# Performance work log

Hardware: AMD Instinct MI355X
Metric: run time of the kernel (lower is better)

The kernel has to match this reference:

```python
import jax, jax.numpy as jnp
import numpy as np

B, L, INPUT_DIM = 2, 2048, 512
D_MODEL, N_HEAD, MLP_HIDDEN = 1024, 16, 4096
CONTEXT_LENGTH = 2048
EPS = 1e-5


def _layer_norm(x, w, b):
    mu = jnp.mean(x, axis=-1, keepdims=True)
    var = jnp.mean(jnp.square(x - mu), axis=-1, keepdims=True)
    return (x - mu) * jax.lax.rsqrt(var + EPS) * w + b


def setup_inputs() -> dict:
    key = jax.random.key(0)
    ks = jax.random.split(key, 12)
    s = 0.02
    return {
        "x": jax.random.normal(ks[0], (B, L, INPUT_DIM), dtype=jnp.float32),
        "wte_w": jax.random.normal(ks[1], (INPUT_DIM, D_MODEL), dtype=jnp.float32) * s,
        "wte_b": jnp.zeros((D_MODEL,), dtype=jnp.float32),
        "wpe": jax.random.normal(ks[2], (CONTEXT_LENGTH, D_MODEL), dtype=jnp.float32) * s,
        "ln1_w": jnp.ones((D_MODEL,), dtype=jnp.float32),
        "ln1_b": jnp.zeros((D_MODEL,), dtype=jnp.float32),
        "kq_w": jax.random.normal(ks[3], (D_MODEL, 2 * D_MODEL), dtype=jnp.float32) * s,
        "kq_b": jnp.zeros((2 * D_MODEL,), dtype=jnp.float32),
        "v_w": jax.random.normal(ks[4], (D_MODEL, D_MODEL), dtype=jnp.float32) * s,
        "v_b": jnp.zeros((D_MODEL,), dtype=jnp.float32),
        "ao_w": jax.random.normal(ks[5], (D_MODEL, D_MODEL), dtype=jnp.float32) * s,
        "ao_b": jnp.zeros((D_MODEL,), dtype=jnp.float32),
        "ln2_w": jnp.ones((D_MODEL,), dtype=jnp.float32),
        "ln2_b": jnp.zeros((D_MODEL,), dtype=jnp.float32),
        "fc_w": jax.random.normal(ks[6], (D_MODEL, MLP_HIDDEN), dtype=jnp.float32) * s,
        "fc_b": jnp.zeros((MLP_HIDDEN,), dtype=jnp.float32),
        "proj_w": jax.random.normal(ks[7], (MLP_HIDDEN, INPUT_DIM), dtype=jnp.float32) * s,
        "proj_b": jnp.zeros((INPUT_DIM,), dtype=jnp.float32),
    }


def reference(x, wte_w, wte_b, wpe, ln1_w, ln1_b, kq_w, kq_b, v_w, v_b,
              ao_w, ao_b, ln2_w, ln2_b, fc_w, fc_b, proj_w, proj_b):
    b, l, _ = x.shape
    hd = D_MODEL // N_HEAD
    # token "embedding" (linear) + learnable positional embedding
    h = x @ wte_w + wte_b + wpe[:l]                      # [B, L, D]
    hn = _layer_norm(h, ln1_w, ln1_b)                    # ln_1
    # attention (kq fused linear -> split gives k first, then q)
    kq = hn @ kq_w + kq_b                                # [B, L, 2D]
    k, q = kq[..., :D_MODEL], kq[..., D_MODEL:]
    v = hn @ v_w + v_b
    q = q.reshape(b, l, N_HEAD, hd).transpose(0, 2, 1, 3)  # [B, H, L, hd]
    k = k.reshape(b, l, N_HEAD, hd).transpose(0, 2, 1, 3)
    v = v.reshape(b, l, N_HEAD, hd).transpose(0, 2, 1, 3)
    scale = 1.0 / jnp.sqrt(jnp.asarray(hd, dtype=q.dtype))
    scores = jnp.einsum('bhqd,bhkd->bhqk', q, k) * scale  # [B, H, L, L]
    causal = jnp.tril(jnp.ones((l, l), dtype=bool))
    scores = jnp.where(causal, scores, jnp.asarray(-jnp.inf, dtype=scores.dtype))
    attn = jax.nn.softmax(scores, axis=-1)
    o = jnp.einsum('bhqk,bhkd->bhqd', attn, v)            # [B, H, L, hd]
    o = o.transpose(0, 2, 1, 3).reshape(b, l, D_MODEL)
    o = o @ ao_w + ao_b
    attn_out = hn + o                                     # residual recorded by Block
    xo = _layer_norm(attn_out, ln2_w, ln2_b)              # ln_2
    # MLP head to input_dim (exact GELU, matching torch nn.GELU default)
    out = jax.nn.gelu(xo @ fc_w + fc_b, approximate=False) @ proj_w + proj_b
    return (out, attn_out)
```

## Files before the change

### kernel.cpp

```cpp
#include <hip/hip_runtime.h>
#include <hip/hip_bf16.h>
#include <cmath>

#define D_MODEL   1024
#define N_HEAD    16
#define HEAD_DIM  64
#define SEQ_LEN   2048
#define NBATCH    2
#define M_TOTAL   (NBATCH * SEQ_LEN)
#define IN_DIM    512
#define MLP_HID   4096

typedef __attribute__((ext_vector_type(8))) short short8;
typedef __attribute__((ext_vector_type(4))) short short4v;
typedef __attribute__((ext_vector_type(4))) float floatx4;

typedef const __attribute__((address_space(1))) void* gas_ptr;
typedef __attribute__((address_space(3))) void* las_ptr;

__device__ __forceinline__ void async_copy16(const void* g, void* l) {
  __builtin_amdgcn_global_load_lds((gas_ptr)g, (las_ptr)l, 16, 0, 0);
}


__global__ __launch_bounds__(256) void k_prep(const float* __restrict__ wte_w,
                                              const float* __restrict__ kq_w,
                                              const float* __restrict__ v_w,
                                              const float* __restrict__ ao_w,
                                              const float* __restrict__ fc_w,
                                              const float* __restrict__ proj_w,
                                              const float* __restrict__ x,
                                              __hip_bfloat16* __restrict__ wT,
                                              __hip_bfloat16* __restrict__ x_bf) {
  const int bid = blockIdx.x;
  const float* in; __hip_bfloat16* out; int K, N, local;
  if (bid < 512)        { in = wte_w;  out = wT;           K = IN_DIM;  N = D_MODEL;     local = bid;        }
  else if (bid < 2560)  { in = kq_w;   out = wT +  524288; K = D_MODEL; N = 2 * D_MODEL; local = bid - 512;  }
  else if (bid < 3584)  { in = v_w;    out = wT + 2621440; K = D_MODEL; N = D_MODEL;     local = bid - 2560; }
  else if (bid < 4608)  { in = ao_w;   out = wT + 3670016; K = D_MODEL; N = D_MODEL;     local = bid - 3584; }
  else if (bid < 8704)  { in = fc_w;   out = wT + 4718592; K = D_MODEL; N = MLP_HID;     local = bid - 4608; }
  else if (bid < 10752) { in = proj_w; out = wT + 8912896; K = MLP_HID; N = IN_DIM;      local = bid - 8704; }
  else {
    int i = (bid - 10752) * 256 + threadIdx.x;
    float4 v = ((const float4*)x)[i];
    short4v o;
    ((__hip_bfloat16*)&o)[0] = __float2bfloat16(v.x);
    ((__hip_bfloat16*)&o)[1] = __float2bfloat16(v.y);
    ((__hip_bfloat16*)&o)[2] = __float2bfloat16(v.z);
    ((__hip_bfloat16*)&o)[3] = __float2bfloat16(v.w);
    ((short4v*)x_bf)[i] = o;
    return;
  }
  __shared__ float tile[32][33];
  const int ntx = N >> 5;
  const int bx = local % ntx, by = local / ntx;
  const int n0 = bx * 32, k0 = by * 32;
  const int tx = threadIdx.x & 31, ty = threadIdx.x >> 5;
#pragma unroll
  for (int i = 0; i < 32; i += 8)
    tile[ty + i][tx] = in[(size_t)(k0 + ty + i) * N + n0 + tx];
  __syncthreads();
#pragma unroll
  for (int i = 0; i < 32; i += 8)
    out[(size_t)(n0 + ty + i) * K + k0 + tx] = __float2bfloat16(tile[tx][ty + i]);
}

__global__ __launch_bounds__(256) void k_reduce_proj(const __hip_bfloat16* __restrict__ part,
                                                     const float* __restrict__ bias,
                                                     float* __restrict__ out) {
  int i = blockIdx.x * 256 + threadIdx.x;
  const size_t SP = (size_t)M_TOTAL * IN_DIM / 4;
  float4 s = ((const float4*)bias)[i & (IN_DIM / 4 - 1)];
#pragma unroll
  for (int j = 0; j < 8; j++) {
    short4v v = ((const short4v*)part)[i + j * SP];
    s.x += __bfloat162float(((const __hip_bfloat16*)&v)[0]);
    s.y += __bfloat162float(((const __hip_bfloat16*)&v)[1]);
    s.z += __bfloat162float(((const __hip_bfloat16*)&v)[2]);
    s.w += __bfloat162float(((const __hip_bfloat16*)&v)[3]);
  }
  ((float4*)out)[i] = s;
}


__global__ __launch_bounds__(256) void k_ln1_combine(const float* __restrict__ part,
                                                     const float* __restrict__ wb,
                                                     const float* __restrict__ wpe,
                                                     const float* __restrict__ lw,
                                                     const float* __restrict__ lb,
                                                     __hip_bfloat16* __restrict__ out_bf) {
  int row = blockIdx.x;
  int l = row & (SEQ_LEN - 1);
  float4 a = ((const float4*)(part + (size_t)row * D_MODEL))[threadIdx.x];
  float4 c = ((const float4*)(part + (size_t)(M_TOTAL + row) * D_MODEL))[threadIdx.x];
  float4 wb4 = ((const float4*)wb)[threadIdx.x];
  float4 pe4 = ((const float4*)(wpe + (size_t)l * D_MODEL))[threadIdx.x];
  float4 v;
  v.x = a.x + c.x + wb4.x + pe4.x;
  v.y = a.y + c.y + wb4.y + pe4.y;
  v.z = a.z + c.z + wb4.z + pe4.z;
  v.w = a.w + c.w + wb4.w + pe4.w;
  float s  = v.x + v.y + v.z + v.w;
  float sq = v.x * v.x + v.y * v.y + v.z * v.z + v.w * v.w;
#pragma unroll
  for (int o = 1; o < 64; o <<= 1) { s += __shfl_xor(s, o); sq += __shfl_xor(sq, o); }
  __shared__ float ss[4], ssq[4];
  int lane = threadIdx.x & 63, wv = threadIdx.x >> 6;
  if (lane == 0) { ss[wv] = s; ssq[wv] = sq; }
  __syncthreads();
  s  = ss[0] + ss[1] + ss[2] + ss[3];
  sq = ssq[0] + ssq[1] + ssq[2] + ssq[3];
  float mu  = s * (1.f / D_MODEL);
  float var = sq * (1.f / D_MODEL) - mu * mu;
  float rs  = rsqrtf(var + 1e-5f);
  float4 lw4 = ((const float4*)lw)[threadIdx.x];
  float4 lb4 = ((const float4*)lb)[threadIdx.x];
  size_t base = (size_t)row * D_MODEL + threadIdx.x * 4;
  out_bf[base + 0] = __float2bfloat16((v.x - mu) * rs * lw4.x + lb4.x);
  out_bf[base + 1] = __float2bfloat16((v.y - mu) * rs * lw4.y + lb4.y);
  out_bf[base + 2] = __float2bfloat16((v.z - mu) * rs * lw4.z + lb4.z);
  out_bf[base + 3] = __float2bfloat16((v.w - mu) * rs * lw4.w + lb4.w);
}

__global__ __launch_bounds__(256) void k_ln2_combine(const float* __restrict__ part,
                                                     const float* __restrict__ bias,
                                                     const __hip_bfloat16* __restrict__ hn,
                                                     const float* __restrict__ lw,
                                                     const float* __restrict__ lb,
                                                     float* __restrict__ attn_out,
                                                     __hip_bfloat16* __restrict__ out_bf) {
  int row = blockIdx.x;
  float4 a = ((const float4*)(part + (size_t)row * D_MODEL))[threadIdx.x];
  float4 c = ((const float4*)(part + (size_t)(M_TOTAL + row) * D_MODEL))[threadIdx.x];
  float4 b4 = ((const float4*)bias)[threadIdx.x];
  short4v h4 = ((const short4v*)(hn + (size_t)row * D_MODEL))[threadIdx.x];
  float4 v;
  v.x = a.x + c.x + b4.x + __bfloat162float(((const __hip_bfloat16*)&h4)[0]);
  v.y = a.y + c.y + b4.y + __bfloat162float(((const __hip_bfloat16*)&h4)[1]);
  v.z = a.z + c.z + b4.z + __bfloat162float(((const __hip_bfloat16*)&h4)[2]);
  v.w = a.w + c.w + b4.w + __bfloat162float(((const __hip_bfloat16*)&h4)[3]);
  ((float4*)(attn_out + (size_t)row * D_MODEL))[threadIdx.x] = v;
  float s  = v.x + v.y + v.z + v.w;
  float sq = v.x * v.x + v.y * v.y + v.z * v.z + v.w * v.w;
#pragma unroll
  for (int o = 1; o < 64; o <<= 1) { s += __shfl_xor(s, o); sq += __shfl_xor(sq, o); }
  __shared__ float ss[4], ssq[4];
  int lane = threadIdx.x & 63, wv = threadIdx.x >> 6;
  if (lane == 0) { ss[wv] = s; ssq[wv] = sq; }
  __syncthreads();
  s  = ss[0] + ss[1] + ss[2] + ss[3];
  sq = ssq[0] + ssq[1] + ssq[2] + ssq[3];
  float mu  = s * (1.f / D_MODEL);
  float var = sq * (1.f / D_MODEL) - mu * mu;
  float rs  = rsqrtf(var + 1e-5f);
  float4 lw4 = ((const float4*)lw)[threadIdx.x];
  float4 lb4 = ((const float4*)lb)[threadIdx.x];
  size_t base = (size_t)row * D_MODEL + threadIdx.x * 4;
  out_bf[base + 0] = __float2bfloat16((v.x - mu) * rs * lw4.x + lb4.x);
  out_bf[base + 1] = __float2bfloat16((v.y - mu) * rs * lw4.y + lb4.y);
  out_bf[base + 2] = __float2bfloat16((v.z - mu) * rs * lw4.z + lb4.z);
  out_bf[base + 3] = __float2bfloat16((v.w - mu) * rs * lw4.w + lb4.w);
}


struct KQVEpi {
  const float* kq_b; const float* v_b;
  __hip_bfloat16* kb; __hip_bfloat16* qb; __hip_bfloat16* vt;
  __device__ void operator()(int row, int col, const floatx4& v) const {
    int b = row >> 11, l = row & (SEQ_LEN - 1);
    int which = col >> 10, c = col & (D_MODEL - 1);
    int head = c >> 6, d = c & 63;
    if (which == 2) {
      float bias = v_b[c];
      short4v o;
#pragma unroll
      for (int t = 0; t < 4; t++)
        ((__hip_bfloat16*)&o)[t] = __float2bfloat16(v[t] + bias);
      *(short4v*)(vt + ((size_t)(b * N_HEAD + head) * HEAD_DIM + d) * SEQ_LEN + l) = o;
    } else {
      float bias = kq_b[col];
      float scale = (which == 1) ? 0.125f : 1.f;
      __hip_bfloat16* dst = (which == 0) ? kb : qb;
#pragma unroll
      for (int t = 0; t < 4; t++)
        dst[((size_t)(b * N_HEAD + head) * SEQ_LEN + l + t) * HEAD_DIM + d] =
            __float2bfloat16((v[t] + bias) * scale);
    }
  }
};

struct FCEpi {
  const float* bias; __hip_bfloat16* act;
  __device__ void operator()(int row, int col, const floatx4& v) const {
    float bi = bias[col];
#pragma unroll
    for (int t = 0; t < 4; t++) {
      float x = v[t] + bi;
      float g = 0.5f * x * (1.f + erff(x * 0.70710678118654752f));
      act[(size_t)(row + t) * MLP_HID + col] = __float2bfloat16(g);
    }
  }
};

struct PartEpi {
  float* part;
  __device__ void operator()(int row, int col, const floatx4& v) const {
    float* p = part + (size_t)blockIdx.z * ((size_t)M_TOTAL * D_MODEL) +
               (size_t)row * D_MODEL + col;
#pragma unroll
    for (int t = 0; t < 4; t++) p[(size_t)t * D_MODEL] = v[t];
  }
};

struct PartBf16Epi {
  __hip_bfloat16* part;
  __device__ void operator()(int row, int col, const floatx4& v) const {
    __hip_bfloat16* p = part + (size_t)blockIdx.z * ((size_t)M_TOTAL * IN_DIM) +
                        (size_t)row * IN_DIM + col;
#pragma unroll
    for (int t = 0; t < 4; t++) p[(size_t)t * IN_DIM] = __float2bfloat16(v[t]);
  }
};


template <class Epi>
__global__ __launch_bounds__(256) void k_gemm(const __hip_bfloat16* __restrict__ A,
                                              const __hip_bfloat16* __restrict__ Bt,
                                              int M, int N, int K, int Kchunk, Epi epi) {
  __shared__ __align__(16) short As[128 * 64];
  __shared__ __align__(16) short Bs[128 * 64];
  const int tid  = threadIdx.x;
  const int lane = tid & 63;
  const int w    = tid >> 6;
  const int wm   = (w >> 1) << 6;
  const int wn   = (w & 1) << 6;
  const int r    = lane & 15;
  const int quad = lane >> 4;
  const int m0 = blockIdx.y << 7;
  const int n0 = blockIdx.x << 7;
  const int koff = blockIdx.z * Kchunk;

  const __hip_bfloat16* pa[4];
  const __hip_bfloat16* pb[4];
#pragma unroll
  for (int j = 0; j < 4; j++) {
    int s = tid + j * 256;
    int row = s >> 3;
    int c = (s & 7) ^ (row & 7);
    pa[j] = A  + (size_t)(m0 + row) * K + (c << 3) + koff;
    pb[j] = Bt + (size_t)(n0 + row) * K + (c << 3) + koff;
  }

  floatx4 acc[4][4];
#pragma unroll
  for (int i = 0; i < 4; i++)
#pragma unroll
    for (int j = 0; j < 4; j++) acc[i][j] = (floatx4){0.f, 0.f, 0.f, 0.f};

  int aoff[2][4], boff[2][4];
#pragma unroll
  for (int kk = 0; kk < 2; kk++)
#pragma unroll
    for (int i = 0; i < 4; i++) {
      int pc = ((quad + (kk << 2)) ^ (r & 7)) << 3;
      aoff[kk][i] = (wm + i * 16 + r) * 64 + pc;
      boff[kk][i] = (wn + i * 16 + r) * 64 + pc;
    }

  for (int k0 = 0; k0 < Kchunk; k0 += 64) {
    __syncthreads();
#pragma unroll
    for (int j = 0; j < 4; j++) {
      async_copy16(pa[j] + k0, &As[(tid + j * 256) * 8]);
      async_copy16(pb[j] + k0, &Bs[(tid + j * 256) * 8]);
    }
    __syncthreads();
#pragma unroll
    for (int kk = 0; kk < 2; kk++) {
      short8 fa[4], fb[4];
#pragma unroll
      for (int i = 0; i < 4; i++) {
        fa[i] = *(const short8*)&As[aoff[kk][i]];
        fb[i] = *(const short8*)&Bs[boff[kk][i]];
      }
#pragma unroll
      for (int i = 0; i < 4; i++)
#pragma unroll
        for (int j = 0; j < 4; j++)
          acc[i][j] = __builtin_amdgcn_mfma_f32_16x16x32_bf16(fa[i], fb[j], acc[i][j], 0, 0, 0);
    }
  }

#pragma unroll
  for (int i = 0; i < 4; i++)
#pragma unroll
    for (int j = 0; j < 4; j++)
      epi(m0 + wm + i * 16 + quad * 4, n0 + wn + j * 16 + r, acc[i][j]);
}

template <class Epi>
static void launch_gemm(const __hip_bfloat16* A, const __hip_bfloat16* Bt,
                        int M, int N, int K, Epi epi, hipStream_t s) {
  dim3 grid(N / 128, M / 128, 1);
  k_gemm<Epi><<<grid, 256, 0, s>>>(A, Bt, M, N, K, K, epi);
}


#define STAGE_A(BUF, H, KT)                                                       \
  do {                                                                            \
    async_copy16(ga + (size_t)((H) * 128) * K + (KT) * 64,                        \
                 &As[BUF][(tid + (H) * 1024) * 8]);                               \
    async_copy16(ga + (size_t)((H) * 128 + 64) * K + (KT) * 64,                   \
                 &As[BUF][(tid + (H) * 1024 + 512) * 8]);                         \
  } while (0)

#define STAGE_B(BUF, H, KT)                                                       \
  do {                                                                            \
    async_copy16(gb + (size_t)((H) * 128) * K + (KT) * 64,                        \
                 &Bs[BUF][(tid + (H) * 1024) * 8]);                               \
    async_copy16(gb + (size_t)((H) * 128 + 64) * K + (KT) * 64,                   \
                 &Bs[BUF][(tid + (H) * 1024 + 512) * 8]);                         \
  } while (0)

#define MFMA_BLK(IO, JO, BFX)                                                     \
  _Pragma("unroll") for (int i = 0; i < 4; i++) {                                 \
    _Pragma("unroll") for (int j = 0; j < 2; j++) {                               \
      acc[(IO) + i][(JO) + j] = __builtin_amdgcn_mfma_f32_16x16x32_bf16(          \
          af[i][0], BFX[j][0], acc[(IO) + i][(JO) + j], 0, 0, 0);                 \
      acc[(IO) + i][(JO) + j] = __builtin_amdgcn_mfma_f32_16x16x32_bf16(          \
          af[i][1], BFX[j][1], acc[(IO) + i][(JO) + j], 0, 0, 0);                 \
    }                                                                             \
  }

#define GTILE(T, BUF)                                                             \
  {                                                                               \
    _Pragma("unroll") for (int i = 0; i < 4; i++) {                               \
      af[i][0] = *(const short8*)&As[BUF][arb[i] + pc0];                          \
      af[i][1] = *(const short8*)&As[BUF][arb[i] + pc1];                          \
    }                                                                             \
    _Pragma("unroll") for (int j = 0; j < 2; j++) {                               \
      bf0[j][0] = *(const short8*)&Bs[BUF][brb[j] + pc0];                         \
      bf0[j][1] = *(const short8*)&Bs[BUF][brb[j] + pc1];                         \
    }                                                                             \
    if ((T) + 1 < nt) { STAGE_A((BUF) ^ 1, 1, (T) + 1); }                         \
    __builtin_amdgcn_s_barrier();                                                 \
    asm volatile("s_waitcnt lgkmcnt(0)" ::: "memory");                            \
    __builtin_amdgcn_s_setprio(1);                                                \
    MFMA_BLK(0, 0, bf0)                                                           \
    __builtin_amdgcn_s_setprio(0);                                                \
    __builtin_amdgcn_s_barrier();                                                 \
    _Pragma("unroll") for (int j = 0; j < 2; j++) {                               \
      bf1[j][0] = *(const short8*)&Bs[BUF][brb[j] + 8192 + pc0];                  \
      bf1[j][1] = *(const short8*)&Bs[BUF][brb[j] + 8192 + pc1];                  \
    }                                                                             \
    if ((T) + 2 < nt) { STAGE_A(BUF, 0, (T) + 2); }                               \
    __builtin_amdgcn_s_barrier();                                                 \
    asm volatile("s_waitcnt lgkmcnt(0)" ::: "memory");                            \
    __builtin_amdgcn_s_setprio(1);                                                \
    MFMA_BLK(0, 2, bf1)                                                           \
    __builtin_amdgcn_s_setprio(0);                                                \
    __builtin_amdgcn_s_barrier();                                                 \
    _Pragma("unroll") for (int i = 0; i < 4; i++) {                               \
      af[i][0] = *(const short8*)&As[BUF][arb[i] + 8192 + pc0];                   \
      af[i][1] = *(const short8*)&As[BUF][arb[i] + 8192 + pc1];                   \
    }                                                                             \
    if ((T) + 2 < nt) { STAGE_B(BUF, 0, (T) + 2); }                               \
    __builtin_amdgcn_s_barrier();                                                 \
    asm volatile("s_waitcnt lgkmcnt(0)" ::: "memory");                            \
    __builtin_amdgcn_s_setprio(1);                                                \
    MFMA_BLK(4, 0, bf0)                                                           \
    __builtin_amdgcn_s_setprio(0);                                                \
    __builtin_amdgcn_s_barrier();                                                 \
    if ((T) + 2 < nt) { STAGE_B(BUF, 1, (T) + 2); }                               \
    __builtin_amdgcn_s_setprio(1);                                                \
    MFMA_BLK(4, 2, bf1)                                                           \
    __builtin_amdgcn_s_setprio(0);                                                \
    if ((T) + 2 < nt) {                                                           \
      asm volatile("s_waitcnt vmcnt(6)" ::: "memory");                            \
    } else {                                                                      \
      asm volatile("s_waitcnt vmcnt(0)" ::: "memory");                            \
    }                                                                             \
    __builtin_amdgcn_s_barrier();                                                 \
  }

template <class Epi>
__global__ __launch_bounds__(512, 2) void k_gemm256(const __hip_bfloat16* __restrict__ A,
                                                    const __hip_bfloat16* __restrict__ Bt,
                                                    int M, int N, int K, int Kchunk, Epi epi) {
  (void)M; (void)N;
  __shared__ __align__(16) short As[2][16384];
  __shared__ __align__(16) short Bs[2][16384];
  const int tid  = threadIdx.x;
  const int lane = tid & 63;
  const int w    = tid >> 6;
  const int wr   = w >> 2;
  const int wc   = w & 3;
  const int r    = lane & 15;
  const int quad = lane >> 4;
  const int m0 = blockIdx.y << 8;
  const int n0 = blockIdx.x << 8;
  const int koff = blockIdx.z * Kchunk;
  const int nt = Kchunk >> 6;

  const int sr = tid >> 3;
  const int sc = (tid & 7) ^ (sr & 7);
  const __hip_bfloat16* ga = A  + (size_t)(m0 + sr) * K + sc * 8 + koff;
  const __hip_bfloat16* gb = Bt + (size_t)(n0 + sr) * K + sc * 8 + koff;

  const int pc0 = ((quad    ) ^ (r & 7)) << 3;
  const int pc1 = ((quad + 4) ^ (r & 7)) << 3;
  int arb[4], brb[2];
#pragma unroll
  for (int i = 0; i < 4; i++) arb[i] = ((2 * i + wr) * 16 + r) * 64;
#pragma unroll
  for (int j = 0; j < 2; j++) brb[j] = ((4 * j + wc) * 16 + r) * 64;

  floatx4 acc[8][4];
#pragma unroll
  for (int i = 0; i < 8; i++)
#pragma unroll
    for (int j = 0; j < 4; j++) acc[i][j] = (floatx4){0.f, 0.f, 0.f, 0.f};
  short8 af[4][2], bf0[2][2], bf1[2][2];

  STAGE_A(0, 0, 0);
  STAGE_B(0, 0, 0);
  STAGE_B(0, 1, 0);
  STAGE_A(0, 1, 0);
  if (nt > 1) {
    STAGE_A(1, 0, 1);
    STAGE_B(1, 0, 1);
    STAGE_B(1, 1, 1);
    asm volatile("s_waitcnt vmcnt(6)" ::: "memory");
  } else {
    asm volatile("s_waitcnt vmcnt(0)" ::: "memory");
  }
  __builtin_amdgcn_s_barrier();

  for (int t = 0; t < nt; t += 2) {
    GTILE(t, 0)
    GTILE(t + 1, 1)
  }

#pragma unroll
  for (int i = 0; i < 8; i++)
#pragma unroll
    for (int j = 0; j < 4; j++)
      epi(m0 + (2 * i + wr) * 16 + quad * 4, n0 + (4 * j + wc) * 16 + r, acc[i][j]);
}


#define PSTR 68

#define STAGE_KV(T, P)                                                         \
  do {                                                                         \
    async_copy16(kp + (size_t)((((T) << 6)) + srow) * HEAD_DIM + sg * 8,       \
                 &Ks[P][tid * 8]);                                             \
    async_copy16(vp + (size_t)srow * SEQ_LEN + ((T) << 6) + sg * 8,            \
                 &Vs[P][tid * 8]);                                             \
  } while (0)

#define ATILE(T, P)                                                            \
  {                                                                            \
    const int ts = (T) << 6;                                                   \
    if (ts < qend) {                                                           \
      _Pragma("unroll") for (int kt = 0; kt < 4; kt++) {                       \
        const int tss = ts + (kt << 4);                                        \
        short4v pk0;                                                           \
        if (tss < qend) {                                                      \
          const int krow = (kt << 4) + r;                                      \
          short8 a0 = *(const short8*)&Ks[P][(krow * 8 + (quad ^ sw)) * 8];    \
          short8 a1 = *(const short8*)&Ks[P][(krow * 8 + ((quad ^ sw) ^ 4)) * 8]; \
          floatx4 s0 = (floatx4){0.f, 0.f, 0.f, 0.f};                          \
          s0 = __builtin_amdgcn_mfma_f32_16x16x32_bf16(a0, qf0, s0, 0, 0, 0);  \
          s0 = __builtin_amdgcn_mfma_f32_16x16x32_bf16(a1, qf1, s0, 0, 0, 0);  \
          if (tss + 15 > qbw) {                                                \
            int off0 = qbw + r - tss;                                          \
            _Pragma("unroll") for (int tt = 0; tt < 4; tt++) {                 \
              int kl = (quad << 2) + tt;                                       \
              if (kl > off0) s0[tt] = -INFINITY;                               \
            }                                                                  \
          }                                                                    \
          _Pragma("unroll") for (int tt = 0; tt < 4; tt++) {                   \
            float e0 = __expf(s0[tt]); ls0 += e0;                              \
            ((__hip_bfloat16*)&pk0)[tt] = __float2bfloat16(e0);                \
          }                                                                    \
        } else {                                                               \
          pk0 = (short4v){0, 0, 0, 0};                                         \
        }                                                                      \
        *(short4v*)(pw + r * PSTR + (kt << 4) + (quad << 2)) = pk0;            \
      }                                                                        \
      __builtin_amdgcn_s_setprio(1);                                           \
      _Pragma("unroll") for (int c = 0; c < 2; c++) {                          \
        short8 pb0 = *(const short8*)(pw + r * PSTR + (c << 5) + (quad << 3)); \
        _Pragma("unroll") for (int fd = 0; fd < 4; fd++) {                     \
          const int vrow = (fd << 4) + r;                                      \
          short8 va = *(const short8*)&Vs[P][(vrow * 8 + (((c << 2) + quad) ^ sw)) * 8]; \
          of[fd] = __builtin_amdgcn_mfma_f32_16x16x32_bf16(va, pb0, of[fd], 0, 0, 0); \
        }                                                                      \
      }                                                                        \
      __builtin_amdgcn_s_setprio(0);                                           \
    }                                                                          \
    __builtin_amdgcn_s_barrier();                                              \
    if ((T) + 2 < ktiles) {                                                    \
      STAGE_KV((T) + 2, P);                                                    \
      asm volatile("s_waitcnt vmcnt(2)" ::: "memory");                         \
    } else {                                                                   \
      asm volatile("s_waitcnt vmcnt(0)" ::: "memory");                         \
    }                                                                          \
    __builtin_amdgcn_s_barrier();                                              \
    __builtin_amdgcn_sched_barrier(0);                                         \
  }

__global__ __launch_bounds__(512, 4) void k_flash_attn(const __hip_bfloat16* __restrict__ kb,
                                                       const __hip_bfloat16* __restrict__ qb,
                                                       const __hip_bfloat16* __restrict__ vtb,
                                                       __hip_bfloat16* __restrict__ ob) {
  __shared__ __align__(16) short Ks[2][64 * 64];
  __shared__ __align__(16) short Vs[2][64 * 64];
  __shared__ __align__(16) __hip_bfloat16 Pb[8][16 * PSTR];
  const int tid  = threadIdx.x;
  const int lane = tid & 63;
  const int w    = tid >> 6;
  const int r    = lane & 15;
  const int quad = lane >> 4;
  const int sw   = r & 7;
  const int bh    = blockIdx.x & 31;
  const int strip = (SEQ_LEN / 128 - 1) - (blockIdx.x >> 5);
  const int qb0   = strip << 7;
  const int qbw   = qb0 + (w << 4);
  const int qend  = qbw + 16;
  const int b = bh >> 4, h = bh & (N_HEAD - 1);

  const __hip_bfloat16* qp = qb  + ((size_t)bh * SEQ_LEN + qbw) * HEAD_DIM;
  const __hip_bfloat16* kp = kb  + (size_t)bh * SEQ_LEN * HEAD_DIM;
  const __hip_bfloat16* vp = vtb + (size_t)bh * HEAD_DIM * SEQ_LEN;
  __hip_bfloat16* pw = &Pb[w][0];

  short8 qf0 = *(const short8*)(qp + r * HEAD_DIM + quad * 8);
  short8 qf1 = *(const short8*)(qp + r * HEAD_DIM + quad * 8 + 32);

  floatx4 of[4];
#pragma unroll
  for (int i = 0; i < 4; i++) of[i] = (floatx4){0.f, 0.f, 0.f, 0.f};
  float ls0 = 0.f;

  const int srow = tid >> 3;
  const int sg = (tid & 7) ^ (srow & 7);

  const int ktiles = (qb0 + 128) >> 6;
  STAGE_KV(0, 0);
  STAGE_KV(1, 1);
  asm volatile("s_waitcnt vmcnt(2)" ::: "memory");
  __builtin_amdgcn_s_barrier();
  __builtin_amdgcn_sched_barrier(0);

  for (int t = 0; t < ktiles; t += 2) {
    ATILE(t, 0)
    ATILE(t + 1, 1)
  }

  ls0 += __shfl_xor(ls0, 16); ls0 += __shfl_xor(ls0, 32);
  float inv0 = 1.f / ls0;

  size_t orow = ((size_t)b * SEQ_LEN + qbw + r) * D_MODEL + (size_t)h * HEAD_DIM;
#pragma unroll
  for (int fd = 0; fd < 4; fd++) {
    short4v o4;
#pragma unroll
    for (int tt = 0; tt < 4; tt++)
      ((__hip_bfloat16*)&o4)[tt] = __float2bfloat16(of[fd][tt] * inv0);
    *(short4v*)(ob + orow + fd * 16 + quad * 4) = o4;
  }
}


extern "C" void kernel_launch(void* const* d_in, const int* in_sizes, int n_in,
                              void* d_out, int out_size, void* d_ws, size_t ws_size,
                              hipStream_t stream) {
  (void)in_sizes; (void)n_in; (void)out_size; (void)ws_size;
  const float* x      = (const float*)d_in[0];
  const float* wte_w  = (const float*)d_in[1];
  const float* wte_b  = (const float*)d_in[2];
  const float* wpe    = (const float*)d_in[3];
  const float* ln1_w  = (const float*)d_in[4];
  const float* ln1_b  = (const float*)d_in[5];
  const float* kq_w   = (const float*)d_in[6];
  const float* kq_b   = (const float*)d_in[7];
  const float* v_w    = (const float*)d_in[8];
  const float* v_b    = (const float*)d_in[9];
  const float* ao_w   = (const float*)d_in[10];
  const float* ao_b   = (const float*)d_in[11];
  const float* ln2_w  = (const float*)d_in[12];
  const float* ln2_b  = (const float*)d_in[13];
  const float* fc_w   = (const float*)d_in[14];
  const float* fc_b   = (const float*)d_in[15];
  const float* proj_w = (const float*)d_in[16];
  const float* proj_b = (const float*)d_in[17];

  float* out0     = (float*)d_out;
  float* attn_out = out0 + (size_t)M_TOTAL * IN_DIM;

  char* ws = (char*)d_ws;
  __hip_bfloat16* wT    = (__hip_bfloat16*)ws;
  __hip_bfloat16* x_bf  = (__hip_bfloat16*)(ws + 22 * 1048576);
  char* R1              = ws + 26 * 1048576;
  float* embed_part     = (float*)R1;
  float* ao_part        = (float*)R1;
  __hip_bfloat16* act   = (__hip_bfloat16*)R1;
  __hip_bfloat16* k_bf  = (__hip_bfloat16*)(ws + 58 * 1048576);
  __hip_bfloat16* q_bf  = (__hip_bfloat16*)(ws + 66 * 1048576);
  __hip_bfloat16* vt_bf = (__hip_bfloat16*)(ws + 74 * 1048576);
  __hip_bfloat16* o_bf  = (__hip_bfloat16*)(ws + 82 * 1048576);
  __hip_bfloat16* hn_bf = (__hip_bfloat16*)(ws + 90 * 1048576);
  __hip_bfloat16* xo_bf = k_bf;
  __hip_bfloat16* proj_part = k_bf;

  __hip_bfloat16* wteT  = wT;
  __hip_bfloat16* kqvT  = wT +  524288;
  __hip_bfloat16* aoT   = wT + 3670016;
  __hip_bfloat16* fcT   = wT + 4718592;
  __hip_bfloat16* projT = wT + 8912896;

  k_prep<<<12800, 256, 0, stream>>>(wte_w, kq_w, v_w, ao_w, fc_w, proj_w, x, wT, x_bf);

  {
    dim3 grid(D_MODEL / 128, M_TOTAL / 128, 2);
    k_gemm<PartEpi><<<grid, 256, 0, stream>>>(x_bf, wteT, M_TOTAL, D_MODEL, IN_DIM, IN_DIM / 2,
                                              PartEpi{embed_part});
  }

  k_ln1_combine<<<M_TOTAL, 256, 0, stream>>>(embed_part, wte_b, wpe, ln1_w, ln1_b, hn_bf);

  launch_gemm(hn_bf, kqvT, M_TOTAL, 3 * D_MODEL, D_MODEL,
              KQVEpi{kq_b, v_b, k_bf, q_bf, vt_bf}, stream);

  k_flash_attn<<<(SEQ_LEN / 128) * 32, 512, 0, stream>>>(k_bf, q_bf, vt_bf, o_bf);

  {
    dim3 grid(D_MODEL / 128, M_TOTAL / 128, 2);
    k_gemm<PartEpi><<<grid, 256, 0, stream>>>(o_bf, aoT, M_TOTAL, D_MODEL, D_MODEL, D_MODEL / 2,
                                              PartEpi{ao_part});
  }

  k_ln2_combine<<<M_TOTAL, 256, 0, stream>>>(ao_part, ao_b, hn_bf, ln2_w, ln2_b, attn_out, xo_bf);

  {
    dim3 grid(MLP_HID / 256, M_TOTAL / 256, 1);
    k_gemm256<FCEpi><<<grid, 512, 0, stream>>>(xo_bf, fcT, M_TOTAL, MLP_HID, D_MODEL, D_MODEL,
                                               FCEpi{fc_b, act});
  }

  {
    dim3 grid(IN_DIM / 256, M_TOTAL / 256, 8);
    k_gemm256<PartBf16Epi><<<grid, 512, 0, stream>>>(act, projT, M_TOTAL, IN_DIM, MLP_HID,
                                                     MLP_HID / 8, PartBf16Epi{proj_part});
  }
  k_reduce_proj<<<M_TOTAL * IN_DIM / 4 / 256, 256, 0, stream>>>(proj_part, proj_b, out0);
}
```

Before: 358.3 us.

## Widen weight transpose tiles, vectorize proj reduction, interleave QK and PV in attention

```diff
diff --git a/kernel.cpp b/kernel.cpp
--- a/kernel.cpp
+++ b/kernel.cpp
@@ -34,14 +34,14 @@
                                               __hip_bfloat16* __restrict__ x_bf) {
   const int bid = blockIdx.x;
   const float* in; __hip_bfloat16* out; int K, N, local;
-  if (bid < 512)        { in = wte_w;  out = wT;           K = IN_DIM;  N = D_MODEL;     local = bid;        }
-  else if (bid < 2560)  { in = kq_w;   out = wT +  524288; K = D_MODEL; N = 2 * D_MODEL; local = bid - 512;  }
-  else if (bid < 3584)  { in = v_w;    out = wT + 2621440; K = D_MODEL; N = D_MODEL;     local = bid - 2560; }
-  else if (bid < 4608)  { in = ao_w;   out = wT + 3670016; K = D_MODEL; N = D_MODEL;     local = bid - 3584; }
-  else if (bid < 8704)  { in = fc_w;   out = wT + 4718592; K = D_MODEL; N = MLP_HID;     local = bid - 4608; }
-  else if (bid < 10752) { in = proj_w; out = wT + 8912896; K = MLP_HID; N = IN_DIM;      local = bid - 8704; }
+  if (bid < 128)        { in = wte_w;  out = wT;           K = IN_DIM;  N = D_MODEL;     local = bid;        }
+  else if (bid < 640)   { in = kq_w;   out = wT +  524288; K = D_MODEL; N = 2 * D_MODEL; local = bid - 128;  }
+  else if (bid < 896)   { in = v_w;    out = wT + 2621440; K = D_MODEL; N = D_MODEL;     local = bid - 640;  }
+  else if (bid < 1152)  { in = ao_w;   out = wT + 3670016; K = D_MODEL; N = D_MODEL;     local = bid - 896;  }
+  else if (bid < 2176)  { in = fc_w;   out = wT + 4718592; K = D_MODEL; N = MLP_HID;     local = bid - 1152; }
+  else if (bid < 2688)  { in = proj_w; out = wT + 8912896; K = MLP_HID; N = IN_DIM;      local = bid - 2176; }
   else {
-    int i = (bid - 10752) * 256 + threadIdx.x;
+    int i = (bid - 2688) * 256 + threadIdx.x;
     float4 v = ((const float4*)x)[i];
     short4v o;
     ((__hip_bfloat16*)&o)[0] = __float2bfloat16(v.x);
@@ -51,35 +51,57 @@
     ((short4v*)x_bf)[i] = o;
     return;
   }
-  __shared__ float tile[32][33];
-  const int ntx = N >> 5;
-  const int bx = local % ntx, by = local / ntx;
-  const int n0 = bx * 32, k0 = by * 32;
-  const int tx = threadIdx.x & 31, ty = threadIdx.x >> 5;
-#pragma unroll
-  for (int i = 0; i < 32; i += 8)
-    tile[ty + i][tx] = in[(size_t)(k0 + ty + i) * N + n0 + tx];
+  __shared__ __hip_bfloat16 t[64][73];
+  const int ntx = N >> 6;
+  const int n0 = (local % ntx) * 64, k0 = (local / ntx) * 64;
+  const int tx = threadIdx.x & 7, ty = threadIdx.x >> 3;
+#pragma unroll
+  for (int i = 0; i < 64; i += 32) {
+    const float* src = in + (size_t)(k0 + ty + i) * N + n0 + tx * 8;
+    float4 v0 = ((const float4*)src)[0];
+    float4 v1 = ((const float4*)src)[1];
+    t[ty + i][tx * 8 + 0] = __float2bfloat16(v0.x);
+    t[ty + i][tx * 8 + 1] = __float2bfloat16(v0.y);
+    t[ty + i][tx * 8 + 2] = __float2bfloat16(v0.z);
+    t[ty + i][tx * 8 + 3] = __float2bfloat16(v0.w);
+    t[ty + i][tx * 8 + 4] = __float2bfloat16(v1.x);
+    t[ty + i][tx * 8 + 5] = __float2bfloat16(v1.y);
+    t[ty + i][tx * 8 + 6] = __float2bfloat16(v1.z);
+    t[ty + i][tx * 8 + 7] = __float2bfloat16(v1.w);
+  }
   __syncthreads();
 #pragma unroll
-  for (int i = 0; i < 32; i += 8)
-    out[(size_t)(n0 + ty + i) * K + k0 + tx] = __float2bfloat16(tile[tx][ty + i]);
+  for (int i = 0; i < 64; i += 32) {
+    int nr = ty + i;
+    short8 o;
+#pragma unroll
+    for (int j = 0; j < 8; j++) ((__hip_bfloat16*)&o)[j] = t[tx * 8 + j][nr];
+    *(short8*)(out + (size_t)(n0 + nr) * K + k0 + tx * 8) = o;
+  }
 }
 
 __global__ __launch_bounds__(256) void k_reduce_proj(const __hip_bfloat16* __restrict__ part,
                                                      const float* __restrict__ bias,
                                                      float* __restrict__ out) {
   int i = blockIdx.x * 256 + threadIdx.x;
-  const size_t SP = (size_t)M_TOTAL * IN_DIM / 4;
-  float4 s = ((const float4*)bias)[i & (IN_DIM / 4 - 1)];
+  const size_t SP8 = (size_t)M_TOTAL * IN_DIM / 8;
+  int cb = (i & (IN_DIM / 8 - 1)) * 2;
+  float4 s0 = ((const float4*)bias)[cb];
+  float4 s1 = ((const float4*)bias)[cb + 1];
 #pragma unroll
   for (int j = 0; j < 8; j++) {
-    short4v v = ((const short4v*)part)[i + j * SP];
-    s.x += __bfloat162float(((const __hip_bfloat16*)&v)[0]);
-    s.y += __bfloat162float(((const __hip_bfloat16*)&v)[1]);
-    s.z += __bfloat162float(((const __hip_bfloat16*)&v)[2]);
-    s.w += __bfloat162float(((const __hip_bfloat16*)&v)[3]);
-  }
-  ((float4*)out)[i] = s;
+    short8 v = ((const short8*)part)[i + j * SP8];
+    s0.x += __bfloat162float(((const __hip_bfloat16*)&v)[0]);
+    s0.y += __bfloat162float(((const __hip_bfloat16*)&v)[1]);
+    s0.z += __bfloat162float(((const __hip_bfloat16*)&v)[2]);
+    s0.w += __bfloat162float(((const __hip_bfloat16*)&v)[3]);
+    s1.x += __bfloat162float(((const __hip_bfloat16*)&v)[4]);
+    s1.y += __bfloat162float(((const __hip_bfloat16*)&v)[5]);
+    s1.z += __bfloat162float(((const __hip_bfloat16*)&v)[6]);
+    s1.w += __bfloat162float(((const __hip_bfloat16*)&v)[7]);
+  }
+  ((float4*)out)[i * 2]     = s0;
+  ((float4*)out)[i * 2 + 1] = s1;
 }
 
 
@@ -459,46 +481,56 @@
                  &Vs[P][tid * 8]);                                             \
   } while (0)
 
+#define QKSUB(KT, P)                                                           \
+  {                                                                            \
+    const int tss = ts + ((KT) << 4);                                          \
+    short4v pk0;                                                               \
+    if (tss < qend) {                                                          \
+      const int krow = ((KT) << 4) + r;                                        \
+      short8 a0 = *(const short8*)&Ks[P][(krow * 8 + (quad ^ sw)) * 8];        \
+      short8 a1 = *(const short8*)&Ks[P][(krow * 8 + ((quad ^ sw) ^ 4)) * 8];  \
+      floatx4 s0 = (floatx4){0.f, 0.f, 0.f, 0.f};                              \
+      s0 = __builtin_amdgcn_mfma_f32_16x16x32_bf16(a0, qf0, s0, 0, 0, 0);      \
+      s0 = __builtin_amdgcn_mfma_f32_16x16x32_bf16(a1, qf1, s0, 0, 0, 0);      \
+      if (tss + 15 > qbw) {                                                    \
+        int off0 = qbw + r - tss;                                              \
+        _Pragma("unroll") for (int tt = 0; tt < 4; tt++) {                     \
+          int kl = (quad << 2) + tt;                                           \
+          if (kl > off0) s0[tt] = -INFINITY;                                   \
+        }                                                                      \
+      }                                                                        \
+      _Pragma("unroll") for (int tt = 0; tt < 4; tt++) {                       \
+        float e0 = __expf(s0[tt]); ls0 += e0;                                  \
+        ((__hip_bfloat16*)&pk0)[tt] = __float2bfloat16(e0);                    \
+      }                                                                        \
+    } else {                                                                   \
+      pk0 = (short4v){0, 0, 0, 0};                                             \
+    }                                                                          \
+    *(short4v*)(pw + r * PSTR + ((KT) << 4) + (quad << 2)) = pk0;              \
+  }
+
+#define PVC(C, P)                                                              \
+  {                                                                            \
+    short8 pb0 = *(const short8*)(pw + r * PSTR + ((C) << 5) + (quad << 3));   \
+    __builtin_amdgcn_s_setprio(1);                                             \
+    _Pragma("unroll") for (int fd = 0; fd < 4; fd++) {                         \
+      const int vrow = (fd << 4) + r;                                          \
+      short8 va = *(const short8*)&Vs[P][(vrow * 8 + ((((C) << 2) + quad) ^ sw)) * 8]; \
+      of[fd] = __builtin_amdgcn_mfma_f32_16x16x32_bf16(va, pb0, of[fd], 0, 0, 0); \
+    }                                                                          \
+    __builtin_amdgcn_s_setprio(0);                                             \
+  }
+
 #define ATILE(T, P)                                                            \
   {                                                                            \
     const int ts = (T) << 6;                                                   \
     if (ts < qend) {                                                           \
-      _Pragma("unroll") for (int kt = 0; kt < 4; kt++) {                       \
-        const int tss = ts + (kt << 4);                                        \
-        short4v pk0;                                                           \
-        if (tss < qend) {                                                      \
-          const int krow = (kt << 4) + r;                                      \
-          short8 a0 = *(const short8*)&Ks[P][(krow * 8 + (quad ^ sw)) * 8];    \
-          short8 a1 = *(const short8*)&Ks[P][(krow * 8 + ((quad ^ sw) ^ 4)) * 8]; \
-          floatx4 s0 = (floatx4){0.f, 0.f, 0.f, 0.f};                          \
-          s0 = __builtin_amdgcn_mfma_f32_16x16x32_bf16(a0, qf0, s0, 0, 0, 0);  \
-          s0 = __builtin_amdgcn_mfma_f32_16x16x32_bf16(a1, qf1, s0, 0, 0, 0);  \
-          if (tss + 15 > qbw) {                                                \
-            int off0 = qbw + r - tss;                                          \
-            _Pragma("unroll") for (int tt = 0; tt < 4; tt++) {                 \
-              int kl = (quad << 2) + tt;                                       \
-              if (kl > off0) s0[tt] = -INFINITY;                               \
-            }                                                                  \
-          }                                                                    \
-          _Pragma("unroll") for (int tt = 0; tt < 4; tt++) {                   \
-            float e0 = __expf(s0[tt]); ls0 += e0;                              \
-            ((__hip_bfloat16*)&pk0)[tt] = __float2bfloat16(e0);                \
-          }                                                                    \
-        } else {                                                               \
-          pk0 = (short4v){0, 0, 0, 0};                                         \
-        }                                                                      \
-        *(short4v*)(pw + r * PSTR + (kt << 4) + (quad << 2)) = pk0;            \
-      }                                                                        \
-      __builtin_amdgcn_s_setprio(1);                                           \
-      _Pragma("unroll") for (int c = 0; c < 2; c++) {                          \
-        short8 pb0 = *(const short8*)(pw + r * PSTR + (c << 5) + (quad << 3)); \
-        _Pragma("unroll") for (int fd = 0; fd < 4; fd++) {                     \
-          const int vrow = (fd << 4) + r;                                      \
-          short8 va = *(const short8*)&Vs[P][(vrow * 8 + (((c << 2) + quad) ^ sw)) * 8]; \
-          of[fd] = __builtin_amdgcn_mfma_f32_16x16x32_bf16(va, pb0, of[fd], 0, 0, 0); \
-        }                                                                      \
-      }                                                                        \
-      __builtin_amdgcn_s_setprio(0);                                           \
+      QKSUB(0, P)                                                              \
+      QKSUB(1, P)                                                              \
+      PVC(0, P)                                                                \
+      QKSUB(2, P)                                                              \
+      QKSUB(3, P)                                                              \
+      PVC(1, P)                                                                \
     }                                                                          \
     __builtin_amdgcn_s_barrier();                                              \
     if ((T) + 2 < ktiles) {                                                    \
@@ -621,7 +653,7 @@
   __hip_bfloat16* fcT   = wT + 4718592;
   __hip_bfloat16* projT = wT + 8912896;
 
-  k_prep<<<12800, 256, 0, stream>>>(wte_w, kq_w, v_w, ao_w, fc_w, proj_w, x, wT, x_bf);
+  k_prep<<<4736, 256, 0, stream>>>(wte_w, kq_w, v_w, ao_w, fc_w, proj_w, x, wT, x_bf);
 
   {
     dim3 grid(D_MODEL / 128, M_TOTAL / 128, 2);
@@ -655,5 +687,5 @@
     k_gemm256<PartBf16Epi><<<grid, 512, 0, stream>>>(act, projT, M_TOTAL, IN_DIM, MLP_HID,
                                                      MLP_HID / 8, PartBf16Epi{proj_part});
   }
-  k_reduce_proj<<<M_TOTAL * IN_DIM / 4 / 256, 256, 0, stream>>>(proj_part, proj_b, out0);
-}
+  k_reduce_proj<<<M_TOTAL * IN_DIM / 8 / 256, 256, 0, stream>>>(proj_part, proj_b, out0);
+}
```

Result: no change. 362.9 us (+1.3%).
